# Kernel tuning notes

Measured on AMD Instinct MI355X. Metric: run time of the kernel, lower is better.

## Reference

```python
import jax, jax.numpy as jnp
import numpy as np

N_BINS = 30
N = 4_000_000
C = 10


def setup_inputs() -> dict:
    key = jax.random.key(0)
    k1, k2 = jax.random.split(key)
    logits = jax.random.normal(k1, (N, C), dtype=jnp.float32) * 3.0
    softmaxes = jax.nn.softmax(logits, axis=1)  # rows sum to 1, as asserted in the torch module
    labels = jax.random.randint(k2, (N,), 0, C, dtype=jnp.int64)
    return {"softmaxes": softmaxes, "labels": labels}


def reference(softmaxes, labels):
    # confidences, predictions = max over classes
    confidences = jnp.max(softmaxes, axis=1)          # [N]
    predictions = jnp.argmax(softmaxes, axis=1)       # [N]
    accuracies = (predictions == labels).astype(jnp.float32)

    # torch loop uses bins (lower, upper]; conf in ((b)/n, (b+1)/n] -> bin b = ceil(conf*n)-1
    # Single-pass histogram instead of O(n_bins*N) masked rescans.
    bin_idx = jnp.clip(jnp.ceil(confidences * N_BINS).astype(jnp.int32) - 1, 0, N_BINS - 1)

    counts = jax.ops.segment_sum(jnp.ones_like(confidences), bin_idx, num_segments=N_BINS)
    sum_conf = jax.ops.segment_sum(confidences, bin_idx, num_segments=N_BINS)
    sum_correct = jax.ops.segment_sum(accuracies, bin_idx, num_segments=N_BINS)

    n_total = jnp.asarray(confidences.shape[0], dtype=jnp.float32)
    counts_safe = jnp.maximum(counts, 1.0)
    avg_conf = sum_conf / counts_safe
    acc_in_bin = sum_correct / counts_safe
    prop_in_bin = counts / n_total

    gaps = jnp.where(counts > 0, jnp.abs(avg_conf - acc_in_bin) * prop_in_bin, 0.0)
    ece = jnp.sum(gaps)
    return ece.reshape(1)  # matches torch.zeros(1) accumulator shape
```

## Files before the change

### kernel.cpp

```cpp
#include <hip/hip_runtime.h>

#define N_BINS 30
#define NCLASS 10


__global__ void ece_zero_ws(unsigned long long* sum_conf,
                            unsigned int* counts,
                            unsigned int* correct) {
    int i = threadIdx.x;
    if (i < N_BINS) {
        sum_conf[i] = 0ull;
        counts[i]   = 0u;
        correct[i]  = 0u;
    }
}

__global__ __launch_bounds__(256) void ece_hist(
        const float* __restrict__ sm,
        const int*   __restrict__ labels,
        int n,
        unsigned long long* __restrict__ g_sumconf,
        unsigned int* __restrict__ g_counts,
        unsigned int* __restrict__ g_correct) {
    __shared__ unsigned long long s_sumconf[N_BINS];
    __shared__ unsigned int s_counts[N_BINS];
    __shared__ unsigned int s_correct[N_BINS];

    for (int i = threadIdx.x; i < N_BINS; i += blockDim.x) {
        s_sumconf[i] = 0ull;
        s_counts[i]  = 0u;
        s_correct[i] = 0u;
    }
    __syncthreads();

    const long long stride = (long long)gridDim.x * blockDim.x;
    for (long long r = (long long)blockIdx.x * blockDim.x + threadIdx.x;
         r < n; r += stride) {
        const float* row = sm + r * NCLASS;
        float2 v0 = *reinterpret_cast<const float2*>(row + 0);
        float2 v1 = *reinterpret_cast<const float2*>(row + 2);
        float2 v2 = *reinterpret_cast<const float2*>(row + 4);
        float2 v3 = *reinterpret_cast<const float2*>(row + 6);
        float2 v4 = *reinterpret_cast<const float2*>(row + 8);

        float v[NCLASS] = {v0.x, v0.y, v1.x, v1.y, v2.x,
                           v2.y, v3.x, v3.y, v4.x, v4.y};

        float conf = v[0];
        int pred = 0;
        #pragma unroll
        for (int j = 1; j < NCLASS; ++j) {
            if (v[j] > conf) { conf = v[j]; pred = j; }
        }

        int lbl = labels[r];
        unsigned int acc = (pred == lbl) ? 1u : 0u;

        int bin = (int)ceilf(conf * (float)N_BINS) - 1;
        bin = min(max(bin, 0), N_BINS - 1);

        unsigned long long fx = (unsigned long long)((double)conf * 4294967296.0);

        atomicAdd(&s_sumconf[bin], fx);
        atomicAdd(&s_counts[bin], 1u);
        atomicAdd(&s_correct[bin], acc);
    }
    __syncthreads();

    for (int i = threadIdx.x; i < N_BINS; i += blockDim.x) {
        if (s_counts[i]) {
            atomicAdd(&g_sumconf[i], s_sumconf[i]);
            atomicAdd(&g_counts[i],  s_counts[i]);
            atomicAdd(&g_correct[i], s_correct[i]);
        }
    }
}

__global__ void ece_final(const unsigned long long* __restrict__ sum_conf,
                          const unsigned int* __restrict__ counts,
                          const unsigned int* __restrict__ correct,
                          float* __restrict__ out,
                          float n_total) {
    if (blockIdx.x == 0 && threadIdx.x == 0) {
        float ece = 0.0f;
        for (int b = 0; b < N_BINS; ++b) {
            unsigned int cnt = counts[b];
            if (cnt > 0u) {
                float fcnt = (float)cnt;
                float avg_conf = (float)((double)sum_conf[b] / 4294967296.0) / fcnt;
                float acc_in_bin = (float)correct[b] / fcnt;
                float prop = fcnt / n_total;
                ece += fabsf(avg_conf - acc_in_bin) * prop;
            }
        }
        out[0] = ece;
    }
}

extern "C" void kernel_launch(void* const* d_in, const int* in_sizes, int n_in,
                              void* d_out, int out_size, void* d_ws, size_t ws_size,
                              hipStream_t stream) {
    const float* sm  = (const float*)d_in[0];
    const int* labels = (const int*)d_in[1];
    const int n = in_sizes[1];

    unsigned long long* g_sumconf = (unsigned long long*)d_ws;
    unsigned int* g_counts  = (unsigned int*)((char*)d_ws + N_BINS * sizeof(unsigned long long));
    unsigned int* g_correct = g_counts + N_BINS;

    ece_zero_ws<<<1, 64, 0, stream>>>(g_sumconf, g_counts, g_correct);

    const int block = 256;
    const int grid = 2048;
    ece_hist<<<grid, block, 0, stream>>>(sm, labels, n, g_sumconf, g_counts, g_correct);

    ece_final<<<1, 64, 0, stream>>>(g_sumconf, g_counts, g_correct,
                                    (float*)d_out, (float)n);
}
```

Baseline: 73.31 us.

## Pack per-bin stats into one 64-bit atomic and process four rows per thread

Conf, count and correct are packed into a single 64-bit word, so each row needs one shared-memory atomic instead of three. Each thread now handles four contiguous rows with float4 and int4 loads, and merges rows that land in the same bin before issuing atomics. The grid now covers the input in one pass with no grid-stride loop, which launches many more blocks and so adds more global atomics. The 16-bit count and correct fields per block and the 20-bit fixed-point conf lower the precision margin and rely on the per-block row count staying small.

```diff
diff --git a/kernel.cpp b/kernel.cpp
--- a/kernel.cpp
+++ b/kernel.cpp
@@ -2,93 +2,120 @@
 
 #define N_BINS 30
 #define NCLASS 10
+#define RPT 4
+#define BLOCK 256
 
 
-__global__ void ece_zero_ws(unsigned long long* sum_conf,
-                            unsigned int* counts,
-                            unsigned int* correct) {
+__global__ void ece_zero_ws(unsigned long long* g_conf, unsigned long long* g_cc) {
     int i = threadIdx.x;
-    if (i < N_BINS) {
-        sum_conf[i] = 0ull;
-        counts[i]   = 0u;
-        correct[i]  = 0u;
-    }
+    if (i < N_BINS) { g_conf[i] = 0ull; g_cc[i] = 0ull; }
 }
 
-__global__ __launch_bounds__(256) void ece_hist(
+__device__ __forceinline__ void row_stats(const float* __restrict__ v,
+                                          int lbl, int& bin,
+                                          unsigned long long& pack) {
+    float conf = v[0];
+    int pred = 0;
+    #pragma unroll
+    for (int j = 1; j < NCLASS; ++j) {
+        if (v[j] > conf) { conf = v[j]; pred = j; }
+    }
+    int b = (int)ceilf(conf * (float)N_BINS) - 1;
+    bin = min(max(b, 0), N_BINS - 1);
+    unsigned int fx = (unsigned int)(conf * 1048576.0f + 0.5f);
+    unsigned long long acc = (pred == lbl) ? 1ull : 0ull;
+    pack = ((unsigned long long)fx << 32) | (1ull << 16) | acc;
+}
+
+__global__ __launch_bounds__(BLOCK) void ece_hist(
         const float* __restrict__ sm,
         const int*   __restrict__ labels,
         int n,
-        unsigned long long* __restrict__ g_sumconf,
-        unsigned int* __restrict__ g_counts,
-        unsigned int* __restrict__ g_correct) {
-    __shared__ unsigned long long s_sumconf[N_BINS];
-    __shared__ unsigned int s_counts[N_BINS];
-    __shared__ unsigned int s_correct[N_BINS];
-
-    for (int i = threadIdx.x; i < N_BINS; i += blockDim.x) {
-        s_sumconf[i] = 0ull;
-        s_counts[i]  = 0u;
-        s_correct[i] = 0u;
-    }
+        unsigned long long* __restrict__ g_conf,
+        unsigned long long* __restrict__ g_cc) {
+    __shared__ unsigned long long s_hist[N_BINS];
+    for (int i = threadIdx.x; i < N_BINS; i += blockDim.x) s_hist[i] = 0ull;
     __syncthreads();
 
-    const long long stride = (long long)gridDim.x * blockDim.x;
-    for (long long r = (long long)blockIdx.x * blockDim.x + threadIdx.x;
-         r < n; r += stride) {
-        const float* row = sm + r * NCLASS;
-        float2 v0 = *reinterpret_cast<const float2*>(row + 0);
-        float2 v1 = *reinterpret_cast<const float2*>(row + 2);
-        float2 v2 = *reinterpret_cast<const float2*>(row + 4);
-        float2 v3 = *reinterpret_cast<const float2*>(row + 6);
-        float2 v4 = *reinterpret_cast<const float2*>(row + 8);
+    const long long r0 = ((long long)blockIdx.x * BLOCK + threadIdx.x) * RPT;
 
-        float v[NCLASS] = {v0.x, v0.y, v1.x, v1.y, v2.x,
-                           v2.y, v3.x, v3.y, v4.x, v4.y};
+    int b0 = -1, b1 = -2, b2 = -3, b3 = -4;
+    unsigned long long p0 = 0, p1 = 0, p2 = 0, p3 = 0;
+    bool v0 = false, v1 = false, v2 = false, v3 = false;
 
-        float conf = v[0];
-        int pred = 0;
+    if (r0 + RPT <= n) {
+        const float4* p = reinterpret_cast<const float4*>(sm + r0 * NCLASS);
+        float v[RPT * NCLASS];
         #pragma unroll
-        for (int j = 1; j < NCLASS; ++j) {
-            if (v[j] > conf) { conf = v[j]; pred = j; }
+        for (int i = 0; i < 10; ++i) {
+            float4 q = p[i];
+            v[4*i+0] = q.x; v[4*i+1] = q.y; v[4*i+2] = q.z; v[4*i+3] = q.w;
         }
+        const int4 lab = *reinterpret_cast<const int4*>(labels + r0);
+        row_stats(v + 0,          lab.x, b0, p0); v0 = true;
+        row_stats(v + NCLASS,     lab.y, b1, p1); v1 = true;
+        row_stats(v + 2*NCLASS,   lab.z, b2, p2); v2 = true;
+        row_stats(v + 3*NCLASS,   lab.w, b3, p3); v3 = true;
+    } else if (r0 < n) {
+        float v[NCLASS];
+        #pragma unroll
+        for (int k = 0; k < RPT; ++k) {
+            if (r0 + k < n) {
+                #pragma unroll
+                for (int j = 0; j < NCLASS; ++j) v[j] = sm[(r0 + k) * NCLASS + j];
+                int lbl = labels[r0 + k];
+                if (k == 0) { row_stats(v, lbl, b0, p0); v0 = true; }
+                if (k == 1) { row_stats(v, lbl, b1, p1); v1 = true; }
+                if (k == 2) { row_stats(v, lbl, b2, p2); v2 = true; }
+                if (k == 3) { row_stats(v, lbl, b3, p3); v3 = true; }
+            }
+        }
+    }
 
-        int lbl = labels[r];
-        unsigned int acc = (pred == lbl) ? 1u : 0u;
+    if (v1 && b1 == b0) { p0 += p1; v1 = false; }
+    if (v2) {
+        if      (b2 == b0)       { p0 += p2; v2 = false; }
+        else if (v1 && b2 == b1) { p1 += p2; v2 = false; }
+    }
+    if (v3) {
+        if      (b3 == b0)       { p0 += p3; v3 = false; }
+        else if (v1 && b3 == b1) { p1 += p3; v3 = false; }
+        else if (v2 && b3 == b2) { p2 += p3; v3 = false; }
+    }
 
-        int bin = (int)ceilf(conf * (float)N_BINS) - 1;
-        bin = min(max(bin, 0), N_BINS - 1);
+    if (v0) atomicAdd(&s_hist[b0], p0);
+    if (v1) atomicAdd(&s_hist[b1], p1);
+    if (v2) atomicAdd(&s_hist[b2], p2);
+    if (v3) atomicAdd(&s_hist[b3], p3);
 
-        unsigned long long fx = (unsigned long long)((double)conf * 4294967296.0);
-
-        atomicAdd(&s_sumconf[bin], fx);
-        atomicAdd(&s_counts[bin], 1u);
-        atomicAdd(&s_correct[bin], acc);
-    }
     __syncthreads();
 
-    for (int i = threadIdx.x; i < N_BINS; i += blockDim.x) {
-        if (s_counts[i]) {
-            atomicAdd(&g_sumconf[i], s_sumconf[i]);
-            atomicAdd(&g_counts[i],  s_counts[i]);
-            atomicAdd(&g_correct[i], s_correct[i]);
+    if (threadIdx.x < N_BINS) {
+        unsigned long long h = s_hist[threadIdx.x];
+        if (h) {
+            unsigned long long fxsum = h >> 32;
+            unsigned long long cnt   = (h >> 16) & 0xFFFFull;
+            unsigned long long acc   = h & 0xFFFFull;
+            atomicAdd(&g_conf[threadIdx.x], fxsum);
+            atomicAdd(&g_cc[threadIdx.x], (cnt << 32) | acc);
         }
     }
 }
 
-__global__ void ece_final(const unsigned long long* __restrict__ sum_conf,
-                          const unsigned int* __restrict__ counts,
-                          const unsigned int* __restrict__ correct,
+__global__ void ece_final(const unsigned long long* __restrict__ g_conf,
+                          const unsigned long long* __restrict__ g_cc,
                           float* __restrict__ out,
                           float n_total) {
     if (blockIdx.x == 0 && threadIdx.x == 0) {
         float ece = 0.0f;
         for (int b = 0; b < N_BINS; ++b) {
-            unsigned int cnt = counts[b];
+            unsigned long long cc = g_cc[b];
+            unsigned int cnt = (unsigned int)(cc >> 32);
+            unsigned int cor = (unsigned int)(cc & 0xFFFFFFFFull);
             if (cnt > 0u) {
                 float fcnt = (float)cnt;
-                float avg_conf = (float)((double)sum_conf[b] / 4294967296.0) / fcnt;
-                float acc_in_bin = (float)correct[b] / fcnt;
+                float avg_conf = (float)((double)g_conf[b] * (1.0 / 1048576.0)) / fcnt;
+                float acc_in_bin = (float)cor / fcnt;
                 float prop = fcnt / n_total;
                 ece += fabsf(avg_conf - acc_in_bin) * prop;
             }
@@ -100,20 +127,18 @@
 extern "C" void kernel_launch(void* const* d_in, const int* in_sizes, int n_in,
                               void* d_out, int out_size, void* d_ws, size_t ws_size,
                               hipStream_t stream) {
-    const float* sm  = (const float*)d_in[0];
+    const float* sm   = (const float*)d_in[0];
     const int* labels = (const int*)d_in[1];
     const int n = in_sizes[1];
 
-    unsigned long long* g_sumconf = (unsigned long long*)d_ws;
-    unsigned int* g_counts  = (unsigned int*)((char*)d_ws + N_BINS * sizeof(unsigned long long));
-    unsigned int* g_correct = g_counts + N_BINS;
+    unsigned long long* g_conf = (unsigned long long*)d_ws;
+    unsigned long long* g_cc   = g_conf + N_BINS;
 
-    ece_zero_ws<<<1, 64, 0, stream>>>(g_sumconf, g_counts, g_correct);
+    ece_zero_ws<<<1, 64, 0, stream>>>(g_conf, g_cc);
 
-    const int block = 256;
-    const int grid = 2048;
-    ece_hist<<<grid, block, 0, stream>>>(sm, labels, n, g_sumconf, g_counts, g_correct);
+    const int rows_per_block = BLOCK * RPT;
+    const int grid = (n + rows_per_block - 1) / rows_per_block;
+    ece_hist<<<grid, BLOCK, 0, stream>>>(sm, labels, n, g_conf, g_cc);
 
-    ece_final<<<1, 64, 0, stream>>>(g_sumconf, g_counts, g_correct,
-                                    (float*)d_out, (float)n);
+    ece_final<<<1, 64, 0, stream>>>(g_conf, g_cc, (float*)d_out, (float)n);
 }
```

New measurement: 105.6 us. 44.0% more time.

## Replace per-bin count/conf/correct atomics with register-accumulated signed gap sums

Applied to the files above, without the earlier changes.

Uses the identity that each bin's gap times its proportion equals |sum(conf - correct)|/N, so only one signed sum per bin is kept. Each thread accumulates that sum in 30 registers with predicated adds instead of issuing shared-memory atomics per row. Results are reduced with wave shuffles and shared memory, and a last-block-done counter finalises the ECE in place of separate zero and final kernels. The cost is extra register pressure and float/fixed-point accumulation precision.

```diff
diff --git a/kernel.cpp b/kernel.cpp
--- a/kernel.cpp
+++ b/kernel.cpp
@@ -2,118 +2,107 @@
 
 #define N_BINS 30
 #define NCLASS 10
+#define BLOCK 256
+#define GRID 2048
 
 
-__global__ void ece_zero_ws(unsigned long long* sum_conf,
-                            unsigned int* counts,
-                            unsigned int* correct) {
-    int i = threadIdx.x;
-    if (i < N_BINS) {
-        sum_conf[i] = 0ull;
-        counts[i]   = 0u;
-        correct[i]  = 0u;
-    }
-}
-
-__global__ __launch_bounds__(256) void ece_hist(
+__global__ __launch_bounds__(BLOCK) void ece_hist(
         const float* __restrict__ sm,
         const int*   __restrict__ labels,
         int n,
-        unsigned long long* __restrict__ g_sumconf,
-        unsigned int* __restrict__ g_counts,
-        unsigned int* __restrict__ g_correct) {
-    __shared__ unsigned long long s_sumconf[N_BINS];
-    __shared__ unsigned int s_counts[N_BINS];
-    __shared__ unsigned int s_correct[N_BINS];
+        unsigned long long* __restrict__ g_sum,
+        unsigned int* __restrict__ done,
+        float* __restrict__ out) {
+    float acc[N_BINS];
+    #pragma unroll
+    for (int b = 0; b < N_BINS; ++b) acc[b] = 0.0f;
 
-    for (int i = threadIdx.x; i < N_BINS; i += blockDim.x) {
-        s_sumconf[i] = 0ull;
-        s_counts[i]  = 0u;
-        s_correct[i] = 0u;
+    const int tid = threadIdx.x;
+    const int gsize = GRID * BLOCK;
+
+    for (int r = blockIdx.x * BLOCK + tid; r < n; r += gsize) {
+        const float* row = sm + (long long)r * NCLASS;
+        float2 q0 = *reinterpret_cast<const float2*>(row + 0);
+        float2 q1 = *reinterpret_cast<const float2*>(row + 2);
+        float2 q2 = *reinterpret_cast<const float2*>(row + 4);
+        float2 q3 = *reinterpret_cast<const float2*>(row + 6);
+        float2 q4 = *reinterpret_cast<const float2*>(row + 8);
+        int lbl = labels[r];
+
+        float v[NCLASS] = {q0.x, q0.y, q1.x, q1.y, q2.x,
+                           q2.y, q3.x, q3.y, q4.x, q4.y};
+        float conf = v[0];
+        int pred = 0;
+        #pragma unroll
+        for (int j = 1; j < NCLASS; ++j)
+            if (v[j] > conf) { conf = v[j]; pred = j; }
+
+        int bin = min(max((int)ceilf(conf * 30.0f) - 1, 0), N_BINS - 1);
+        float d = conf - ((pred == lbl) ? 1.0f : 0.0f);
+
+        #pragma unroll
+        for (int b = 0; b < N_BINS; ++b)
+            acc[b] += (bin == b) ? d : 0.0f;
+    }
+
+    #pragma unroll
+    for (int b = 0; b < N_BINS; ++b) {
+        float s = acc[b];
+        s += __shfl_xor(s, 1);
+        s += __shfl_xor(s, 2);
+        s += __shfl_xor(s, 4);
+        s += __shfl_xor(s, 8);
+        s += __shfl_xor(s, 16);
+        s += __shfl_xor(s, 32);
+        acc[b] = s;
+    }
+
+    __shared__ float s_part[4][N_BINS];
+    __shared__ unsigned int s_last;
+    const int lane = tid & 63;
+    const int wid  = tid >> 6;
+    if (lane == 0) {
+        #pragma unroll
+        for (int b = 0; b < N_BINS; ++b) s_part[wid][b] = acc[b];
     }
     __syncthreads();
 
-    const long long stride = (long long)gridDim.x * blockDim.x;
-    for (long long r = (long long)blockIdx.x * blockDim.x + threadIdx.x;
-         r < n; r += stride) {
-        const float* row = sm + r * NCLASS;
-        float2 v0 = *reinterpret_cast<const float2*>(row + 0);
-        float2 v1 = *reinterpret_cast<const float2*>(row + 2);
-        float2 v2 = *reinterpret_cast<const float2*>(row + 4);
-        float2 v3 = *reinterpret_cast<const float2*>(row + 6);
-        float2 v4 = *reinterpret_cast<const float2*>(row + 8);
-
-        float v[NCLASS] = {v0.x, v0.y, v1.x, v1.y, v2.x,
-                           v2.y, v3.x, v3.y, v4.x, v4.y};
-
-        float conf = v[0];
-        int pred = 0;
-        #pragma unroll
-        for (int j = 1; j < NCLASS; ++j) {
-            if (v[j] > conf) { conf = v[j]; pred = j; }
-        }
-
-        int lbl = labels[r];
-        unsigned int acc = (pred == lbl) ? 1u : 0u;
-
-        int bin = (int)ceilf(conf * (float)N_BINS) - 1;
-        bin = min(max(bin, 0), N_BINS - 1);
-
-        unsigned long long fx = (unsigned long long)((double)conf * 4294967296.0);
-
-        atomicAdd(&s_sumconf[bin], fx);
-        atomicAdd(&s_counts[bin], 1u);
-        atomicAdd(&s_correct[bin], acc);
+    if (tid < N_BINS) {
+        float s = s_part[0][tid] + s_part[1][tid] + s_part[2][tid] + s_part[3][tid];
+        long long fx = (long long)llrintf(s * 1048576.0f);
+        atomicAdd(&g_sum[tid], (unsigned long long)fx);
     }
+    __threadfence();
     __syncthreads();
 
-    for (int i = threadIdx.x; i < N_BINS; i += blockDim.x) {
-        if (s_counts[i]) {
-            atomicAdd(&g_sumconf[i], s_sumconf[i]);
-            atomicAdd(&g_counts[i],  s_counts[i]);
-            atomicAdd(&g_correct[i], s_correct[i]);
+    if (tid == 0)
+        s_last = (atomicAdd(done, 1u) == GRID - 1) ? 1u : 0u;
+    __syncthreads();
+
+    if (s_last && tid == 0) {
+        __threadfence();
+        double total = 0.0;
+        #pragma unroll
+        for (int b = 0; b < N_BINS; ++b) {
+            long long v = (long long)atomicAdd(&g_sum[b], 0ull);
+            total += fabs((double)v);
         }
-    }
-}
-
-__global__ void ece_final(const unsigned long long* __restrict__ sum_conf,
-                          const unsigned int* __restrict__ counts,
-                          const unsigned int* __restrict__ correct,
-                          float* __restrict__ out,
-                          float n_total) {
-    if (blockIdx.x == 0 && threadIdx.x == 0) {
-        float ece = 0.0f;
-        for (int b = 0; b < N_BINS; ++b) {
-            unsigned int cnt = counts[b];
-            if (cnt > 0u) {
-                float fcnt = (float)cnt;
-                float avg_conf = (float)((double)sum_conf[b] / 4294967296.0) / fcnt;
-                float acc_in_bin = (float)correct[b] / fcnt;
-                float prop = fcnt / n_total;
-                ece += fabsf(avg_conf - acc_in_bin) * prop;
-            }
-        }
-        out[0] = ece;
+        out[0] = (float)(total * (1.0 / 1048576.0) / (double)n);
     }
 }
 
 extern "C" void kernel_launch(void* const* d_in, const int* in_sizes, int n_in,
                               void* d_out, int out_size, void* d_ws, size_t ws_size,
                               hipStream_t stream) {
-    const float* sm  = (const float*)d_in[0];
+    const float* sm   = (const float*)d_in[0];
     const int* labels = (const int*)d_in[1];
     const int n = in_sizes[1];
 
-    unsigned long long* g_sumconf = (unsigned long long*)d_ws;
-    unsigned int* g_counts  = (unsigned int*)((char*)d_ws + N_BINS * sizeof(unsigned long long));
-    unsigned int* g_correct = g_counts + N_BINS;
+    unsigned long long* g_sum = (unsigned long long*)d_ws;
+    unsigned int* done = (unsigned int*)(g_sum + N_BINS);
 
-    ece_zero_ws<<<1, 64, 0, stream>>>(g_sumconf, g_counts, g_correct);
-
-    const int block = 256;
-    const int grid = 2048;
-    ece_hist<<<grid, block, 0, stream>>>(sm, labels, n, g_sumconf, g_counts, g_correct);
-
-    ece_final<<<1, 64, 0, stream>>>(g_sumconf, g_counts, g_correct,
-                                    (float*)d_out, (float)n);
+    hipMemsetAsync(d_ws, 0, N_BINS * sizeof(unsigned long long) + sizeof(unsigned int),
+                   stream);
+    ece_hist<<<GRID, BLOCK, 0, stream>>>(sm, labels, n, g_sum, done,
+                                         (float*)d_out);
 }
```

Measured after the change: 208.6 us. +184.5%, slower.
